# Kernel optimization log

Hardware: AMD Instinct MI355X
Metric: run time of the kernel (lower is better)

The kernel has to match this reference:

```python
import jax, jax.numpy as jnp
import numpy as np

N = 100000   # nodes
E = 1600000  # edges (avg degree 16)
D = 128      # embed_dim
H1, C1 = 8, 16   # gat1: heads=8, out=embed_dim//8=16, concat -> 128
C2 = 32          # gat2: heads=1, out=32
NEG_SLOPE = 0.2  # PyG GATConv default leaky relu slope


def _gat_layer(x, src, dst, W, a_src, a_dst, b, heads, ch, concat):
    """PyG-style GATConv (eval mode, add_self_loops already applied via src/dst)."""
    n = x.shape[0]
    h = (x @ W).reshape(n, heads, ch)                      # [N,H,C]
    alpha_s = jnp.einsum('nhc,hc->nh', h, a_src)           # [N,H]
    alpha_d = jnp.einsum('nhc,hc->nh', h, a_dst)           # [N,H]
    e = jax.nn.leaky_relu(alpha_s[src] + alpha_d[dst], NEG_SLOPE)  # [Etot,H]
    # segment softmax over incoming edges of each dst node
    m = jax.ops.segment_max(e, dst, num_segments=n)        # [N,H]
    ex = jnp.exp(e - m[dst])
    s = jax.ops.segment_sum(ex, dst, num_segments=n)       # [N,H]
    alpha = ex / (s[dst] + 1e-16)                          # [Etot,H]
    out = jax.ops.segment_sum(alpha[:, :, None] * h[src], dst, num_segments=n)  # [N,H,C]
    out = out.reshape(n, heads * ch) if concat else out.mean(axis=1)
    return out + b


def setup_inputs():
    key = jax.random.key(0)
    ks = jax.random.split(key, 12)
    x = jax.random.normal(ks[0], (N, D), dtype=jnp.float32)
    edge_index = jax.random.randint(ks[1], (2, E), 0, N, dtype=jnp.int64)
    sc = 0.1
    W1 = jax.random.normal(ks[2], (D, H1 * C1), jnp.float32) * sc
    a1_src = jax.random.normal(ks[3], (H1, C1), jnp.float32) * sc
    a1_dst = jax.random.normal(ks[4], (H1, C1), jnp.float32) * sc
    b1 = jnp.zeros((H1 * C1,), jnp.float32)
    W2 = jax.random.normal(ks[5], (H1 * C1, C2), jnp.float32) * sc
    a2_src = jax.random.normal(ks[6], (1, C2), jnp.float32) * sc
    a2_dst = jax.random.normal(ks[7], (1, C2), jnp.float32) * sc
    b2 = jnp.zeros((C2,), jnp.float32)
    Wh = jax.random.normal(ks[8], (C2, 1), jnp.float32) * sc
    bh = jnp.zeros((1,), jnp.float32)
    return {"x": x, "edge_index": edge_index,
            "W1": W1, "a1_src": a1_src, "a1_dst": a1_dst, "b1": b1,
            "W2": W2, "a2_src": a2_src, "a2_dst": a2_dst, "b2": b2,
            "Wh": Wh, "bh": bh}


def reference(x, edge_index, W1, a1_src, a1_dst, b1, W2, a2_src, a2_dst, b2, Wh, bh):
    n = x.shape[0]
    loops = jnp.arange(n, dtype=edge_index.dtype)
    src = jnp.concatenate([edge_index[0], loops])  # add_self_loops=True (PyG default)
    dst = jnp.concatenate([edge_index[1], loops])
    h = jax.nn.elu(_gat_layer(x, src, dst, W1, a1_src, a1_dst, b1, H1, C1, True))
    h = jax.nn.elu(_gat_layer(h, src, dst, W2, a2_src, a2_dst, b2, 1, C2, False))
    return h @ Wh + bh  # [N,1] ordinal head
```

## Files before the change

### kernel.cpp

```cpp
#include <hip/hip_runtime.h>
#include <hip/hip_bf16.h>
#include <stdint.h>
#include <stddef.h>

#define NEG_SLOPE 0.2f
#define XS 136

#define NBK   196
#define BWSH  9
#define BCAP  12288
#define NPREP 64

typedef __bf16 bf16x8 __attribute__((ext_vector_type(8)));
typedef float  f32x4  __attribute__((ext_vector_type(4)));

__device__ __forceinline__ float bf2f(__hip_bfloat16 b){ return __bfloat162float(b); }
__device__ __forceinline__ float lo_bf(unsigned u){ return __uint_as_float(u << 16); }
__device__ __forceinline__ float hi_bf(unsigned u){ return __uint_as_float(u & 0xffff0000u); }
__device__ __forceinline__ float lrelu(float u){ return fmaxf(u, NEG_SLOPE * u); }
__device__ __forceinline__ unsigned short f2bf(float f){
    unsigned u = __float_as_uint(f);
    return (unsigned short)((u + 0x7fffu + ((u >> 16) & 1u)) >> 16);
}
__device__ __forceinline__ float bfs2f(unsigned short s){ return __uint_as_float((unsigned)s << 16); }
__device__ __forceinline__ float ldraw(const void* p, int i, int isf){
    return isf ? ((const float*)p)[i] : bf2f(((const __hip_bfloat16*)p)[i]);
}

__global__ void detect_kernel(const unsigned* __restrict__ ei,
                              const unsigned* __restrict__ xw,
                              int* __restrict__ flags,
                              int* __restrict__ gcur){
    __shared__ int vote;
    const int t = threadIdx.x;
    if (t == 0) vote = 0;
    if (t < NBK) gcur[t] = t * BCAP;
    __syncthreads();
    if (t < 64){
        unsigned long long m = __ballot(ei[2*t + 1] != 0u);
        if (t == 0) flags[0] = (m == 0ull) ? 1 : 0;
    }
    {
        unsigned lo = xw[t] & 0xffffu;
        unsigned e  = (lo >> 7) & 0xffu;
        int pl = ((lo & 0x7fffu) == 0u || (e >= 100u && e <= 140u)) ? 1 : 0;
        atomicAdd(&vote, pl);
    }
    __syncthreads();
    if (t == 0) flags[1] = (vote < 128) ? 1 : 0;
}

#define WTS_TOTAL 20993
__global__ __launch_bounds__(256) void prep_scatter_kernel(
        const void* __restrict__ ei, const int* __restrict__ flags,
        int* __restrict__ gcur, unsigned* __restrict__ pairs, int E, int Et, int nsb,
        const void* W1, const void* W2, const void* a1s, const void* a1d,
        const void* b1, const void* a2s, const void* a2d, const void* b2,
        const void* Wh, const void* bh,
        float* __restrict__ w, unsigned short* __restrict__ w1x,
        unsigned short* __restrict__ w2x){
    const int t = threadIdx.x;
    if ((int)blockIdx.x < nsb){
        __shared__ int cnt[NBK], base[NBK], lcnt[NBK];
        const int e0 = blockIdx.x * 4096;
        const int nE = min(4096, Et - e0);
        for (int i = t; i < NBK; i += 256){ cnt[i] = 0; lcnt[i] = 0; }
        __syncthreads();
        const int is64 = flags[0];
        int2 sd[16];
#pragma unroll
        for (int k = 0; k < 16; k++){
            int j = t + k * 256;
            if (j < nE){
                int e = e0 + j, s, d;
                if (e >= E){ s = e - E; d = s; }
                else if (is64){
                    const long long* p = (const long long*)ei;
                    s = (int)p[e]; d = (int)p[(size_t)E + e];
                } else {
                    const int* p = (const int*)ei;
                    s = p[e]; d = p[(size_t)E + e];
                }
                sd[k] = make_int2(s, d);
                atomicAdd(&cnt[d >> BWSH], 1);
            } else sd[k].y = -1;
        }
        __syncthreads();
        for (int b = t; b < NBK; b += 256)
            base[b] = cnt[b] ? atomicAdd(&gcur[b], cnt[b]) : 0;
        __syncthreads();
#pragma unroll
        for (int k = 0; k < 16; k++){
            if (sd[k].y >= 0){
                int b = sd[k].y >> BWSH;
                int r = atomicAdd(&lcnt[b], 1);
                pairs[(size_t)base[b] + r] = ((unsigned)sd[k].x << BWSH) | (unsigned)(sd[k].y & 511);
            }
        }
    } else {
        const int p   = blockIdx.x - nsb;
        const int tid = p * 256 + t;
        const int NT  = NPREP * 256;
        const int isf = flags[1];
        for (int i = tid; i < 513; i += NT){
            int gi = 20480 + i;
            const void* src; int off;
            if      (gi < 20608){ src = a1s; off = gi - 20480; }
            else if (gi < 20736){ src = a1d; off = gi - 20608; }
            else if (gi < 20864){ src = b1;  off = gi - 20736; }
            else if (gi < 20896){ src = a2s; off = gi - 20864; }
            else if (gi < 20928){ src = a2d; off = gi - 20896; }
            else if (gi < 20960){ src = b2;  off = gi - 20928; }
            else if (gi < 20992){ src = Wh;  off = gi - 20960; }
            else                { src = bh;  off = 0; }
            w[gi] = ldraw(src, off, isf);
        }
        for (int i = tid; i < 16384; i += NT){
            int c = i >> 7, k = i & 127;
            w1x[i] = f2bf(ldraw(W1, k*128 + c, isf));
        }
        for (int i = tid; i < 4096; i += NT){
            int c = i >> 7, k = i & 127;
            w2x[i] = f2bf(ldraw(W2, k*32 + c, isf));
        }
        for (int i = tid; i < 12*128; i += NT) w2x[36*128 + i] = 0;
        for (int i = tid; i < 1024; i += NT){
            int h = i >> 7, k = i & 127;
            float ss = 0.f, dd = 0.f;
#pragma unroll
            for (int j = 0; j < 16; j++){
                float hv = ldraw(W1, k*128 + h*16 + j, isf);
                ss += hv * ldraw(a1s, h*16 + j, isf);
                dd += hv * ldraw(a1d, h*16 + j, isf);
            }
            unsigned short sh = f2bf(ss), dh = f2bf(dd);
            w1x[(128+h)*128 + k] = sh;
            w1x[(136+h)*128 + k] = f2bf(ss - bfs2f(sh));
            w1x[(144+h)*128 + k] = dh;
            w1x[(152+h)*128 + k] = f2bf(dd - bfs2f(dh));
        }
        for (int k = tid; k < 128; k += NT){
            float ss = 0.f, dd = 0.f;
#pragma unroll
            for (int j = 0; j < 32; j++){
                float hv = ldraw(W2, k*32 + j, isf);
                ss += hv * ldraw(a2s, j, isf);
                dd += hv * ldraw(a2d, j, isf);
            }
            unsigned short sh = f2bf(ss), dh = f2bf(dd);
            w2x[32*128 + k] = sh;
            w2x[33*128 + k] = f2bf(ss - bfs2f(sh));
            w2x[34*128 + k] = dh;
            w2x[35*128 + k] = f2bf(dd - bfs2f(dh));
        }
    }
}

__global__ __launch_bounds__(256) void g1csr_kernel(
        const unsigned* __restrict__ pairs, const int* __restrict__ gcur,
        int* __restrict__ rowptr, int* __restrict__ csr_src, int Nn,
        const void* __restrict__ xv, const unsigned short* __restrict__ w1x,
        const int* __restrict__ flags, __hip_bfloat16* __restrict__ h1b,
        float* __restrict__ as1, float* __restrict__ ad1){
    __shared__ __align__(16) char smem[52224];
    const int t = threadIdx.x;
    if ((int)blockIdx.x < NBK){
        int* ssz   = (int*)smem;
        int* sscan = ssz + 256;
        int* cnt   = sscan + 256;
        int* sh    = cnt + 512;
        const int b = blockIdx.x;
        int v = (t < NBK) ? (gcur[t] - t * BCAP) : 0;
        ssz[t] = v; sscan[t] = v;
        __syncthreads();
        for (int off = 1; off < 256; off <<= 1){
            int x = (t >= off) ? sscan[t - off] : 0;
            __syncthreads();
            sscan[t] += x;
            __syncthreads();
        }
        const int sz = ssz[b];
        const int eb = (b == 0) ? 0 : sscan[b - 1];
        if (b == 0 && t == 0) rowptr[Nn] = sscan[NBK - 1];
        const unsigned* pp = pairs + (size_t)b * BCAP;
        cnt[t] = 0; cnt[t + 256] = 0;
        __syncthreads();
        for (int i = t; i < sz; i += 256) atomicAdd(&cnt[pp[i] & 511u], 1);
        __syncthreads();
        int l0 = 2*t, l1 = 2*t + 1;
        int s0 = cnt[l0], s1 = cnt[l1], ts = s0 + s1;
        sh[t] = ts; __syncthreads();
        for (int off = 1; off < 256; off <<= 1){
            int x = (t >= off) ? sh[t - off] : 0;
            __syncthreads();
            sh[t] += x;
            __syncthreads();
        }
        int excl = sh[t] - ts;
        __syncthreads();
        cnt[l0] = eb + excl;
        cnt[l1] = eb + excl + s0;
        int n0 = (b << BWSH) + l0, n1 = (b << BWSH) + l1;
        if (n0 < Nn) rowptr[n0] = cnt[l0];
        if (n1 < Nn) rowptr[n1] = cnt[l1];
        __syncthreads();
        for (int i = t; i < sz; i += 256){
            unsigned sd = pp[i];
            int pos = atomicAdd(&cnt[sd & 511u], 1);
            csr_src[pos] = (int)(sd >> BWSH);
        }
    } else {
        __bf16* xls = (__bf16*)smem;
        __bf16* wls = (__bf16*)(smem + 64 * XS * 2);
        const int row0 = ((int)blockIdx.x - NBK) * 64;
        const int n = Nn;

#pragma unroll
        for (int k = 0; k < 8; k++){
            int e = (t + k * 256) * 8;
            int c = e >> 7, kk = e & 127;
            *(uint4*)(&wls[c * XS + kk]) = *(const uint4*)(w1x + e);
        }
        if (row0 + 64 <= n){
            if (flags[1]){
                const float* xp = (const float*)xv + (size_t)row0 * 128;
#pragma unroll
                for (int k = 0; k < 8; k++){
                    int e = (t + k * 256) * 4;
                    int row = e >> 7, col = e & 127;
                    float4 vv = *(const float4*)(xp + e);
                    uint2 o;
                    o.x = (unsigned)f2bf(vv.x) | ((unsigned)f2bf(vv.y) << 16);
                    o.y = (unsigned)f2bf(vv.z) | ((unsigned)f2bf(vv.w) << 16);
                    *(uint2*)(&xls[row * XS + col]) = o;
                }
            } else {
                const unsigned short* xp = (const unsigned short*)xv + (size_t)row0 * 128;
#pragma unroll
                for (int k = 0; k < 4; k++){
                    int e = (t + k * 256) * 8;
                    int row = e >> 7, col = e & 127;
                    *(uint4*)(&xls[row * XS + col]) = *(const uint4*)(xp + e);
                }
            }
        } else {
            const int limit = (n - row0) * 128;
            if (flags[1]){
                const float* xp = (const float*)xv + (size_t)row0 * 128;
                for (int i = t; i < 64 * 128; i += 256){
                    float v = (i < limit) ? xp[i] : 0.f;
                    xls[(i >> 7) * XS + (i & 127)] = (__bf16)v;
                }
            } else {
                const unsigned short* xp = (const unsigned short*)xv + (size_t)row0 * 128;
                for (int i = t; i < 64 * 128; i += 256){
                    unsigned short v = (i < limit) ? xp[i] : (unsigned short)0;
                    ((unsigned short*)xls)[(i >> 7) * XS + (i & 127)] = v;
                }
            }
        }
        __syncthreads();

        const int w    = t >> 6;
        const int lane = t & 63;
        const int l15  = lane & 15;
        const int quad = lane >> 4;

        f32x4 acc[8] = {};
        f32x4 accS = {}, accD = {};
        const __bf16* xbase = &xls[(w * 16 + l15) * XS + quad * 8];
        const __bf16* wbase = &wls[l15 * XS + quad * 8];
        const unsigned short* vsrow = w1x + (128 + l15) * 128 + quad * 8;
        const unsigned short* vdrow = w1x + (144 + l15) * 128 + quad * 8;

#pragma unroll
        for (int ks = 0; ks < 4; ks++){
            bf16x8 af = *(const bf16x8*)(xbase + ks * 32);
#pragma unroll
            for (int tt = 0; tt < 8; tt++){
                bf16x8 bfr = *(const bf16x8*)(wbase + tt * 16 * XS + ks * 32);
                acc[tt] = __builtin_amdgcn_mfma_f32_16x16x32_bf16(af, bfr, acc[tt], 0, 0, 0);
            }
            bf16x8 bS = *(const bf16x8*)(vsrow + ks * 32);
            bf16x8 bD = *(const bf16x8*)(vdrow + ks * 32);
            accS = __builtin_amdgcn_mfma_f32_16x16x32_bf16(af, bS, accS, 0, 0, 0);
            accD = __builtin_amdgcn_mfma_f32_16x16x32_bf16(af, bD, accD, 0, 0, 0);
        }

#pragma unroll
        for (int tt = 0; tt < 8; tt++){
            int col = tt * 16 + l15;
#pragma unroll
            for (int r = 0; r < 4; r++){
                int row = row0 + w * 16 + quad * 4 + r;
                if (row < n) h1b[(size_t)row * 128 + col] = __float2bfloat16(acc[tt][r]);
            }
        }
#pragma unroll
        for (int r = 0; r < 4; r++){
            float vs = accS[r] + __shfl_xor(accS[r], 8);
            float vd = accD[r] + __shfl_xor(accD[r], 8);
            int row = row0 + w * 16 + quad * 4 + r;
            if (l15 < 8 && row < n){
                as1[(size_t)row * 8 + l15] = vs;
                ad1[(size_t)row * 8 + l15] = vd;
            }
        }
    }
}

__global__ __launch_bounds__(256) void gather1_kernel(const int* __restrict__ rowptr,
                                                      const int* __restrict__ csr_src,
                                                      const float* __restrict__ as1,
                                                      const float* __restrict__ ad1,
                                                      const unsigned* __restrict__ h1u,
                                                      const float* __restrict__ b1,
                                                      unsigned* __restrict__ out1u, int n){
    int wid = blockIdx.x * 4 + (threadIdx.x >> 6);
    if (wid >= n) return;
    const int lane = threadIdx.x & 63;
    const int q    = lane >> 4;
    const int l15  = lane & 15;
    const int h    = l15 >> 1;
    const int start = rowptr[wid], end = rowptr[wid + 1];
    const float adv = ad1[(size_t)wid * 8 + h];
    float den = 0.f;
    float num[8] = {0.f,0.f,0.f,0.f,0.f,0.f,0.f,0.f};
    for (int j = start + q; j < end; j += 4){
        int src = csr_src[j];
        float u = lrelu(as1[(size_t)src * 8 + h] + adv);
        float w = __expf(u);
        uint4 hv = *(const uint4*)(h1u + (size_t)src * 64 + (l15 << 2));
        den += w;
        num[0] += w * lo_bf(hv.x); num[1] += w * hi_bf(hv.x);
        num[2] += w * lo_bf(hv.y); num[3] += w * hi_bf(hv.y);
        num[4] += w * lo_bf(hv.z); num[5] += w * hi_bf(hv.z);
        num[6] += w * lo_bf(hv.w); num[7] += w * hi_bf(hv.w);
    }
    den += __shfl_xor(den, 16); den += __shfl_xor(den, 32);
#pragma unroll
    for (int k = 0; k < 8; k++){
        num[k] += __shfl_xor(num[k], 16);
        num[k] += __shfl_xor(num[k], 32);
    }
    if (lane < 16){
        const int ch0 = l15 * 8;
        float inv = 1.f / (den + 1e-16f);
        uint4 o;
        unsigned* op = (unsigned*)&o;
#pragma unroll
        for (int k = 0; k < 4; k++){
            float r0 = num[2*k]   * inv + b1[ch0 + 2*k];
            float r1 = num[2*k+1] * inv + b1[ch0 + 2*k + 1];
            r0 = r0 > 0.f ? r0 : __expf(r0) - 1.f;
            r1 = r1 > 0.f ? r1 : __expf(r1) - 1.f;
            op[k] = (unsigned)f2bf(r0) | ((unsigned)f2bf(r1) << 16);
        }
        *(uint4*)(out1u + (size_t)wid * 64 + (l15 << 2)) = o;
    }
}

__global__ __launch_bounds__(256) void gemm2_kernel(const unsigned* __restrict__ out1u,
                                                    const unsigned short* __restrict__ w2x,
                                                    __hip_bfloat16* __restrict__ h2b,
                                                    float* __restrict__ as2,
                                                    float* __restrict__ ad2, int n){
    __shared__ __align__(16) __bf16 als[64 * XS];
    __shared__ __align__(16) __bf16 wls[32 * XS];
    const int t = threadIdx.x;
    const int row0 = blockIdx.x * 64;

#pragma unroll
    for (int k = 0; k < 2; k++){
        int e = (t + k * 256) * 8;
        int c = e >> 7, kk = e & 127;
        *(uint4*)(&wls[c * XS + kk]) = *(const uint4*)(w2x + e);
    }
    if (row0 + 64 <= n){
#pragma unroll
        for (int k = 0; k < 4; k++){
            int e = (t + k * 256) * 4;
            int row = e >> 6, cu = e & 63;
            *(uint4*)(&((unsigned*)als)[row * 68 + cu]) =
                *(const uint4*)(out1u + (size_t)row0 * 64 + e);
        }
    } else {
        const int limit = (n - row0) * 64;
        for (int i = t; i < 64 * 64; i += 256){
            unsigned v = (i < limit) ? out1u[(size_t)row0 * 64 + i] : 0u;
            ((unsigned*)als)[(i >> 6) * 68 + (i & 63)] = v;
        }
    }
    __syncthreads();

    const int w    = t >> 6;
    const int lane = t & 63;
    const int l15  = lane & 15;
    const int quad = lane >> 4;

    f32x4 acc[2] = {};
    f32x4 accE = {};
    const __bf16* abase = &als[(w * 16 + l15) * XS + quad * 8];
    const __bf16* bbase = &wls[l15 * XS + quad * 8];
    const unsigned short* verow = w2x + (32 + l15) * 128 + quad * 8;

#pragma unroll
    for (int ks = 0; ks < 4; ks++){
        bf16x8 af = *(const bf16x8*)(abase + ks * 32);
#pragma unroll
        for (int tt = 0; tt < 2; tt++){
            bf16x8 bfr = *(const bf16x8*)(bbase + tt * 16 * XS + ks * 32);
            acc[tt] = __builtin_amdgcn_mfma_f32_16x16x32_bf16(af, bfr, acc[tt], 0, 0, 0);
        }
        bf16x8 bE = *(const bf16x8*)(verow + ks * 32);
        accE = __builtin_amdgcn_mfma_f32_16x16x32_bf16(af, bE, accE, 0, 0, 0);
    }

#pragma unroll
    for (int r = 0; r < 4; r++){
        int row = row0 + w * 16 + quad * 4 + r;
        if (row < n){
#pragma unroll
            for (int tt = 0; tt < 2; tt++){
                int col = tt * 16 + l15;
                h2b[(size_t)row * 32 + col] = __float2bfloat16(acc[tt][r]);
            }
        }
        float vE = accE[r] + __shfl_xor(accE[r], 1);
        if (row < n){
            if (l15 == 0) as2[row] = vE;
            if (l15 == 2) ad2[row] = vE;
        }
    }
}

__global__ __launch_bounds__(256) void gather2_kernel(const int* __restrict__ rowptr,
                                                      const int* __restrict__ csr_src,
                                                      const float* __restrict__ as2,
                                                      const float* __restrict__ ad2,
                                                      const unsigned* __restrict__ h2u,
                                                      const float* __restrict__ b2,
                                                      const float* __restrict__ Wh,
                                                      const float* __restrict__ bh,
                                                      const int* __restrict__ flags,
                                                      void* __restrict__ out, int n){
    int wid = blockIdx.x * 4 + (threadIdx.x >> 6);
    if (wid >= n) return;
    int lane = threadIdx.x & 63;
    int q    = lane >> 4;
    int i2   = lane & 15;
    int ch0  = i2 * 2;
    int start = rowptr[wid], end = rowptr[wid + 1];
    float adv = ad2[wid];
    float den = 0.f, num0 = 0.f, num1 = 0.f;
    for (int j = start + q; j < end; j += 4){
        int src = csr_src[j];
        float u = lrelu(as2[src] + adv);
        float w = __expf(u);
        unsigned hv = h2u[(size_t)src * 16 + i2];
        den += w;
        num0 += w * lo_bf(hv);
        num1 += w * hi_bf(hv);
    }
    den  += __shfl_xor(den, 16);  den  += __shfl_xor(den, 32);
    num0 += __shfl_xor(num0, 16); num0 += __shfl_xor(num0, 32);
    num1 += __shfl_xor(num1, 16); num1 += __shfl_xor(num1, 32);
    float inv = 1.f / (den + 1e-16f);
    float v0 = num0 * inv + b2[ch0];
    float v1 = num1 * inv + b2[ch0 + 1];
    v0 = v0 > 0.f ? v0 : __expf(v0) - 1.f;
    v1 = v1 > 0.f ? v1 : __expf(v1) - 1.f;
    float p = v0 * Wh[ch0] + v1 * Wh[ch0 + 1];
#pragma unroll
    for (int off = 1; off < 16; off <<= 1) p += __shfl_xor(p, off);
    if (lane == 0){
        float r = p + bh[0];
        if (flags[1]) ((float*)out)[wid] = r;
        else          ((__hip_bfloat16*)out)[wid] = __float2bfloat16(r);
    }
}

extern "C" void kernel_launch(void* const* d_in, const int* in_sizes, int n_in,
                              void* d_out, int out_size, void* d_ws, size_t ws_size,
                              hipStream_t stream){
    const void* x   = d_in[0];
    const void* ei  = d_in[1];

    const int Nn = in_sizes[0] / 128;
    const int Ee = in_sizes[1] / 2;
    const int Et = Ee + Nn;
    const int nsb = (Et + 4095) / 4096;

    char* ws = (char*)d_ws;
    auto al = [](size_t v){ return (v + 255) & ~(size_t)255; };
    size_t off = 0;
    int*      flags  = (int*)(ws + off);      off = al(off + 16);
    float*    wts    = (float*)(ws + off);    off = al(off + (size_t)WTS_TOTAL * 4);
    unsigned short* w1x = (unsigned short*)(ws + off); off = al(off + 160 * 128 * 2);
    unsigned short* w2x = (unsigned short*)(ws + off); off = al(off + 48 * 128 * 2);
    int*      gcur   = (int*)(ws + off);      off = al(off + (size_t)NBK * 4);
    int*      rowptr = (int*)(ws + off);      off = al(off + (size_t)(Nn + 1) * 4);
    int*      csrs   = (int*)(ws + off);      off = al(off + (size_t)Et * 4);
    unsigned* pairs  = (unsigned*)(ws + off); off = al(off + (size_t)NBK * BCAP * 4);
    size_t o_h1 = off;
    __hip_bfloat16* h1b = (__hip_bfloat16*)(ws + off); off = al(off + (size_t)Nn * 128 * 2);
    float* as1  = (float*)(ws + off); off = al(off + (size_t)Nn * 8 * 4);
    float* ad1  = (float*)(ws + off); off = al(off + (size_t)Nn * 8 * 4);
    unsigned* out1u = (unsigned*)(ws + off); off = al(off + (size_t)Nn * 128 * 2);
    size_t o2 = o_h1;
    __hip_bfloat16* h2b = (__hip_bfloat16*)(ws + o2); o2 += (size_t)Nn * 32 * 2;
    float* as2  = (float*)(ws + o2);  o2 += (size_t)Nn * 4;
    float* ad2  = (float*)(ws + o2);  o2 += (size_t)Nn * 4;

    float* b1f  = wts + 20736;
    float* b2f  = wts + 20928;
    float* Whf  = wts + 20960;
    float* bhf  = wts + 20992;

    detect_kernel<<<1, 256, 0, stream>>>((const unsigned*)ei, (const unsigned*)x, flags, gcur);

    prep_scatter_kernel<<<nsb + NPREP, 256, 0, stream>>>(ei, flags, gcur, pairs, Ee, Et, nsb,
        d_in[2], d_in[6], d_in[3], d_in[4], d_in[5], d_in[7], d_in[8], d_in[9],
        d_in[10], d_in[11], wts, w1x, w2x);

    g1csr_kernel<<<NBK + (Nn + 63) / 64, 256, 0, stream>>>(pairs, gcur, rowptr, csrs, Nn,
        x, w1x, flags, h1b, as1, ad1);

    gather1_kernel<<<(Nn + 3) / 4, 256, 0, stream>>>(rowptr, csrs, as1, ad1,
                                                     (const unsigned*)h1b, b1f, out1u, Nn);

    gemm2_kernel<<<(Nn + 63) / 64, 256, 0, stream>>>(out1u, w2x, h2b, as2, ad2, Nn);

    gather2_kernel<<<(Nn + 3) / 4, 256, 0, stream>>>(rowptr, csrs, as2, ad2,
                                                     (const unsigned*)h2b, b2f,
                                                     Whf, bhf, flags, d_out, Nn);
}
```

Baseline: 313.1 us.

## Fuse layer-2 linear into gather1 and fold detect kernel into prep

After: 339.4 us. 8.4% more time.

```diff
diff --git a/kernel.cpp b/kernel.cpp
--- a/kernel.cpp
+++ b/kernel.cpp
@@ -10,6 +10,7 @@
 #define BWSH  9
 #define BCAP  12288
 #define NPREP 64
+#define W2S   34
 
 typedef __bf16 bf16x8 __attribute__((ext_vector_type(8)));
 typedef float  f32x4  __attribute__((ext_vector_type(4)));
@@ -27,32 +28,10 @@
     return isf ? ((const float*)p)[i] : bf2f(((const __hip_bfloat16*)p)[i]);
 }
 
-__global__ void detect_kernel(const unsigned* __restrict__ ei,
-                              const unsigned* __restrict__ xw,
-                              int* __restrict__ flags,
-                              int* __restrict__ gcur){
-    __shared__ int vote;
-    const int t = threadIdx.x;
-    if (t == 0) vote = 0;
-    if (t < NBK) gcur[t] = t * BCAP;
-    __syncthreads();
-    if (t < 64){
-        unsigned long long m = __ballot(ei[2*t + 1] != 0u);
-        if (t == 0) flags[0] = (m == 0ull) ? 1 : 0;
-    }
-    {
-        unsigned lo = xw[t] & 0xffffu;
-        unsigned e  = (lo >> 7) & 0xffu;
-        int pl = ((lo & 0x7fffu) == 0u || (e >= 100u && e <= 140u)) ? 1 : 0;
-        atomicAdd(&vote, pl);
-    }
-    __syncthreads();
-    if (t == 0) flags[1] = (vote < 128) ? 1 : 0;
-}
-
 #define WTS_TOTAL 20993
 __global__ __launch_bounds__(256) void prep_scatter_kernel(
-        const void* __restrict__ ei, const int* __restrict__ flags,
+        const void* __restrict__ ei, const unsigned* __restrict__ xw,
+        int* __restrict__ flags,
         int* __restrict__ gcur, unsigned* __restrict__ pairs, int E, int Et, int nsb,
         const void* W1, const void* W2, const void* a1s, const void* a1d,
         const void* b1, const void* a2s, const void* a2d, const void* b2,
@@ -62,11 +41,16 @@
     const int t = threadIdx.x;
     if ((int)blockIdx.x < nsb){
         __shared__ int cnt[NBK], base[NBK], lcnt[NBK];
+        __shared__ int s64;
+        if (t < 64){
+            unsigned long long m = __ballot(((const unsigned*)ei)[2*t + 1] != 0u);
+            if (t == 0) s64 = (m == 0ull) ? 1 : 0;
+        }
         const int e0 = blockIdx.x * 4096;
         const int nE = min(4096, Et - e0);
         for (int i = t; i < NBK; i += 256){ cnt[i] = 0; lcnt[i] = 0; }
         __syncthreads();
-        const int is64 = flags[0];
+        const int is64 = s64;
         int2 sd[16];
 #pragma unroll
         for (int k = 0; k < 16; k++){
@@ -87,7 +71,7 @@
         }
         __syncthreads();
         for (int b = t; b < NBK; b += 256)
-            base[b] = cnt[b] ? atomicAdd(&gcur[b], cnt[b]) : 0;
+            base[b] = cnt[b] ? (b * BCAP + atomicAdd(&gcur[b], cnt[b])) : 0;
         __syncthreads();
 #pragma unroll
         for (int k = 0; k < 16; k++){
@@ -98,10 +82,26 @@
             }
         }
     } else {
+        __shared__ int vote;
+        __shared__ int sflag;
+        if (t == 0) vote = 0;
+        __syncthreads();
+        {
+            unsigned lo = xw[t] & 0xffffu;
+            unsigned e  = (lo >> 7) & 0xffu;
+            int pl = ((lo & 0x7fffu) == 0u || (e >= 100u && e <= 140u)) ? 1 : 0;
+            atomicAdd(&vote, pl);
+        }
+        __syncthreads();
+        if (t == 0){
+            sflag = (vote < 128) ? 1 : 0;
+            if ((int)blockIdx.x == nsb){ flags[0] = 0; flags[1] = sflag; }
+        }
+        __syncthreads();
+        const int isf = sflag;
         const int p   = blockIdx.x - nsb;
         const int tid = p * 256 + t;
         const int NT  = NPREP * 256;
-        const int isf = flags[1];
         for (int i = tid; i < 513; i += NT){
             int gi = 20480 + i;
             const void* src; int off;
@@ -115,15 +115,12 @@
             else                { src = bh;  off = 0; }
             w[gi] = ldraw(src, off, isf);
         }
+        for (int i = tid; i < 4096; i += NT)
+            w[16384 + i] = ldraw(W2, i, isf);
         for (int i = tid; i < 16384; i += NT){
             int c = i >> 7, k = i & 127;
             w1x[i] = f2bf(ldraw(W1, k*128 + c, isf));
         }
-        for (int i = tid; i < 4096; i += NT){
-            int c = i >> 7, k = i & 127;
-            w2x[i] = f2bf(ldraw(W2, k*32 + c, isf));
-        }
-        for (int i = tid; i < 12*128; i += NT) w2x[36*128 + i] = 0;
         for (int i = tid; i < 1024; i += NT){
             int h = i >> 7, k = i & 127;
             float ss = 0.f, dd = 0.f;
@@ -138,20 +135,6 @@
             w1x[(136+h)*128 + k] = f2bf(ss - bfs2f(sh));
             w1x[(144+h)*128 + k] = dh;
             w1x[(152+h)*128 + k] = f2bf(dd - bfs2f(dh));
-        }
-        for (int k = tid; k < 128; k += NT){
-            float ss = 0.f, dd = 0.f;
-#pragma unroll
-            for (int j = 0; j < 32; j++){
-                float hv = ldraw(W2, k*32 + j, isf);
-                ss += hv * ldraw(a2s, j, isf);
-                dd += hv * ldraw(a2d, j, isf);
-            }
-            unsigned short sh = f2bf(ss), dh = f2bf(dd);
-            w2x[32*128 + k] = sh;
-            w2x[33*128 + k] = f2bf(ss - bfs2f(sh));
-            w2x[34*128 + k] = dh;
-            w2x[35*128 + k] = f2bf(dd - bfs2f(dh));
         }
     }
 }
@@ -170,7 +153,7 @@
         int* cnt   = sscan + 256;
         int* sh    = cnt + 512;
         const int b = blockIdx.x;
-        int v = (t < NBK) ? (gcur[t] - t * BCAP) : 0;
+        int v = (t < NBK) ? gcur[t] : 0;
         ssz[t] = v; sscan[t] = v;
         __syncthreads();
         for (int off = 1; off < 256; off <<= 1){
@@ -315,14 +298,32 @@
                                                       const float* __restrict__ ad1,
                                                       const unsigned* __restrict__ h1u,
                                                       const float* __restrict__ b1,
-                                                      unsigned* __restrict__ out1u, int n){
-    int wid = blockIdx.x * 4 + (threadIdx.x >> 6);
-    if (wid >= n) return;
-    const int lane = threadIdx.x & 63;
+                                                      const float* __restrict__ W2f,
+                                                      const float* __restrict__ a2blk,
+                                                      __hip_bfloat16* __restrict__ h2b,
+                                                      float* __restrict__ as2,
+                                                      float* __restrict__ ad2, int n){
+    __shared__ __align__(16) unsigned short w2ls[128 * W2S];
+    __shared__ float a2ls[64];
+    __shared__ __align__(16) float o1f[4 * 128];
+    const int t = threadIdx.x;
+    for (int i = t; i < 4096; i += 256){
+        int k = i >> 5, c = i & 31;
+        w2ls[k * W2S + c] = f2bf(W2f[i]);
+    }
+    if (t < 64) a2ls[t] = a2blk[t];
+    __syncthreads();
+
+    const int wv   = t >> 6;
+    const int lane = t & 63;
+    const int wid0 = blockIdx.x * 4 + wv;
+    const bool active = wid0 < n;
+    const int wid = active ? wid0 : 0;
     const int q    = lane >> 4;
     const int l15  = lane & 15;
     const int h    = l15 >> 1;
-    const int start = rowptr[wid], end = rowptr[wid + 1];
+    const int start = active ? rowptr[wid] : 0;
+    const int end   = active ? rowptr[wid + 1] : 0;
     const float adv = ad1[(size_t)wid * 8 + h];
     float den = 0.f;
     float num[8] = {0.f,0.f,0.f,0.f,0.f,0.f,0.f,0.f};
@@ -346,91 +347,40 @@
     if (lane < 16){
         const int ch0 = l15 * 8;
         float inv = 1.f / (den + 1e-16f);
-        uint4 o;
-        unsigned* op = (unsigned*)&o;
-#pragma unroll
-        for (int k = 0; k < 4; k++){
-            float r0 = num[2*k]   * inv + b1[ch0 + 2*k];
-            float r1 = num[2*k+1] * inv + b1[ch0 + 2*k + 1];
-            r0 = r0 > 0.f ? r0 : __expf(r0) - 1.f;
-            r1 = r1 > 0.f ? r1 : __expf(r1) - 1.f;
-            op[k] = (unsigned)f2bf(r0) | ((unsigned)f2bf(r1) << 16);
-        }
-        *(uint4*)(out1u + (size_t)wid * 64 + (l15 << 2)) = o;
-    }
-}
-
-__global__ __launch_bounds__(256) void gemm2_kernel(const unsigned* __restrict__ out1u,
-                                                    const unsigned short* __restrict__ w2x,
-                                                    __hip_bfloat16* __restrict__ h2b,
-                                                    float* __restrict__ as2,
-                                                    float* __restrict__ ad2, int n){
-    __shared__ __align__(16) __bf16 als[64 * XS];
-    __shared__ __align__(16) __bf16 wls[32 * XS];
-    const int t = threadIdx.x;
-    const int row0 = blockIdx.x * 64;
-
-#pragma unroll
-    for (int k = 0; k < 2; k++){
-        int e = (t + k * 256) * 8;
-        int c = e >> 7, kk = e & 127;
-        *(uint4*)(&wls[c * XS + kk]) = *(const uint4*)(w2x + e);
-    }
-    if (row0 + 64 <= n){
-#pragma unroll
-        for (int k = 0; k < 4; k++){
-            int e = (t + k * 256) * 4;
-            int row = e >> 6, cu = e & 63;
-            *(uint4*)(&((unsigned*)als)[row * 68 + cu]) =
-                *(const uint4*)(out1u + (size_t)row0 * 64 + e);
-        }
-    } else {
-        const int limit = (n - row0) * 64;
-        for (int i = t; i < 64 * 64; i += 256){
-            unsigned v = (i < limit) ? out1u[(size_t)row0 * 64 + i] : 0u;
-            ((unsigned*)als)[(i >> 6) * 68 + (i & 63)] = v;
-        }
-    }
-    __syncthreads();
-
-    const int w    = t >> 6;
-    const int lane = t & 63;
-    const int l15  = lane & 15;
-    const int quad = lane >> 4;
-
-    f32x4 acc[2] = {};
-    f32x4 accE = {};
-    const __bf16* abase = &als[(w * 16 + l15) * XS + quad * 8];
-    const __bf16* bbase = &wls[l15 * XS + quad * 8];
-    const unsigned short* verow = w2x + (32 + l15) * 128 + quad * 8;
-
-#pragma unroll
-    for (int ks = 0; ks < 4; ks++){
-        bf16x8 af = *(const bf16x8*)(abase + ks * 32);
-#pragma unroll
-        for (int tt = 0; tt < 2; tt++){
-            bf16x8 bfr = *(const bf16x8*)(bbase + tt * 16 * XS + ks * 32);
-            acc[tt] = __builtin_amdgcn_mfma_f32_16x16x32_bf16(af, bfr, acc[tt], 0, 0, 0);
-        }
-        bf16x8 bE = *(const bf16x8*)(verow + ks * 32);
-        accE = __builtin_amdgcn_mfma_f32_16x16x32_bf16(af, bE, accE, 0, 0, 0);
-    }
-
-#pragma unroll
-    for (int r = 0; r < 4; r++){
-        int row = row0 + w * 16 + quad * 4 + r;
-        if (row < n){
-#pragma unroll
-            for (int tt = 0; tt < 2; tt++){
-                int col = tt * 16 + l15;
-                h2b[(size_t)row * 32 + col] = __float2bfloat16(acc[tt][r]);
-            }
-        }
-        float vE = accE[r] + __shfl_xor(accE[r], 1);
-        if (row < n){
-            if (l15 == 0) as2[row] = vE;
-            if (l15 == 2) ad2[row] = vE;
-        }
+        float r[8];
+#pragma unroll
+        for (int k = 0; k < 8; k++){
+            float v = num[k] * inv + b1[ch0 + k];
+            r[k] = v > 0.f ? v : __expf(v) - 1.f;
+        }
+        float4* dst = (float4*)&o1f[wv * 128 + ch0];
+        dst[0] = make_float4(r[0], r[1], r[2], r[3]);
+        dst[1] = make_float4(r[4], r[5], r[6], r[7]);
+    }
+    const int c    = lane & 31;
+    const int half = lane >> 5;
+    const float* o1p = &o1f[wv * 128 + half * 64];
+    const unsigned short* wp = &w2ls[(half * 64) * W2S + c];
+    float acc2 = 0.f;
+#pragma unroll
+    for (int j4 = 0; j4 < 16; j4++){
+        float4 ov = *(const float4*)(o1p + j4 * 4);
+        acc2 += ov.x * bfs2f(wp[(j4*4 + 0) * W2S]);
+        acc2 += ov.y * bfs2f(wp[(j4*4 + 1) * W2S]);
+        acc2 += ov.z * bfs2f(wp[(j4*4 + 2) * W2S]);
+        acc2 += ov.w * bfs2f(wp[(j4*4 + 3) * W2S]);
+    }
+    acc2 += __shfl_xor(acc2, 32);
+    float vs = acc2 * a2ls[c];
+    float vd = acc2 * a2ls[32 + c];
+#pragma unroll
+    for (int off = 1; off < 32; off <<= 1){
+        vs += __shfl_xor(vs, off);
+        vd += __shfl_xor(vd, off);
+    }
+    if (active){
+        if (lane < 32) h2b[(size_t)wid * 32 + c] = __float2bfloat16(acc2);
+        if (lane == 0){ as2[wid] = vs; ad2[wid] = vd; }
     }
 }
 
@@ -497,39 +447,37 @@
     int*      flags  = (int*)(ws + off);      off = al(off + 16);
     float*    wts    = (float*)(ws + off);    off = al(off + (size_t)WTS_TOTAL * 4);
     unsigned short* w1x = (unsigned short*)(ws + off); off = al(off + 160 * 128 * 2);
-    unsigned short* w2x = (unsigned short*)(ws + off); off = al(off + 48 * 128 * 2);
     int*      gcur   = (int*)(ws + off);      off = al(off + (size_t)NBK * 4);
     int*      rowptr = (int*)(ws + off);      off = al(off + (size_t)(Nn + 1) * 4);
     int*      csrs   = (int*)(ws + off);      off = al(off + (size_t)Et * 4);
     unsigned* pairs  = (unsigned*)(ws + off); off = al(off + (size_t)NBK * BCAP * 4);
-    size_t o_h1 = off;
     __hip_bfloat16* h1b = (__hip_bfloat16*)(ws + off); off = al(off + (size_t)Nn * 128 * 2);
     float* as1  = (float*)(ws + off); off = al(off + (size_t)Nn * 8 * 4);
     float* ad1  = (float*)(ws + off); off = al(off + (size_t)Nn * 8 * 4);
-    unsigned* out1u = (unsigned*)(ws + off); off = al(off + (size_t)Nn * 128 * 2);
-    size_t o2 = o_h1;
-    __hip_bfloat16* h2b = (__hip_bfloat16*)(ws + o2); o2 += (size_t)Nn * 32 * 2;
-    float* as2  = (float*)(ws + o2);  o2 += (size_t)Nn * 4;
-    float* ad2  = (float*)(ws + o2);  o2 += (size_t)Nn * 4;
-
+    __hip_bfloat16* h2b = (__hip_bfloat16*)(ws + off); off = al(off + (size_t)Nn * 32 * 2);
+    float* as2  = (float*)(ws + off); off = al(off + (size_t)Nn * 4);
+    float* ad2  = (float*)(ws + off); off = al(off + (size_t)Nn * 4);
+
+    float* W2f  = wts + 16384;
     float* b1f  = wts + 20736;
+    float* a2blk= wts + 20864;
     float* b2f  = wts + 20928;
     float* Whf  = wts + 20960;
     float* bhf  = wts + 20992;
 
-    detect_kernel<<<1, 256, 0, stream>>>((const unsigned*)ei, (const unsigned*)x, flags, gcur);
-
-    prep_scatter_kernel<<<nsb + NPREP, 256, 0, stream>>>(ei, flags, gcur, pairs, Ee, Et, nsb,
+    hipMemsetAsync(gcur, 0, (size_t)NBK * 4, stream);
+
+    prep_scatter_kernel<<<nsb + NPREP, 256, 0, stream>>>(ei, (const unsigned*)x, flags,
+        gcur, pairs, Ee, Et, nsb,
         d_in[2], d_in[6], d_in[3], d_in[4], d_in[5], d_in[7], d_in[8], d_in[9],
-        d_in[10], d_in[11], wts, w1x, w2x);
+        d_in[10], d_in[11], wts, w1x, (unsigned short*)nullptr);
 
     g1csr_kernel<<<NBK + (Nn + 63) / 64, 256, 0, stream>>>(pairs, gcur, rowptr, csrs, Nn,
         x, w1x, flags, h1b, as1, ad1);
 
     gather1_kernel<<<(Nn + 3) / 4, 256, 0, stream>>>(rowptr, csrs, as1, ad1,
-                                                     (const unsigned*)h1b, b1f, out1u, Nn);
-
-    gemm2_kernel<<<(Nn + 63) / 64, 256, 0, stream>>>(out1u, w2x, h2b, as2, ad2, Nn);
+                                                     (const unsigned*)h1b, b1f,
+                                                     W2f, a2blk, h2b, as2, ad2, Nn);
 
     gather2_kernel<<<(Nn + 3) / 4, 256, 0, stream>>>(rowptr, csrs, as2, ad2,
                                                      (const unsigned*)h2b, b2f,
```
